# Kernel optimization log

Hardware: AMD Instinct MI355X
Metric: run time of the kernel (lower is better)

The kernel has to match this reference:

```python
import jax, jax.numpy as jnp
import numpy as np

SIZE = 1024
SIZE_INTERNAL = 4096
B, S = 8, 2048
EPS = 1e-5


def layer_norm(x, g, b):
    mu = jnp.mean(x, axis=-1, keepdims=True)
    var = jnp.mean(jnp.square(x - mu), axis=-1, keepdims=True)
    return (x - mu) * jax.lax.rsqrt(var + EPS) * g + b


def setup_inputs() -> dict:
    key = jax.random.key(0)
    ks = jax.random.split(key, 12)
    s = 0.02
    return {
        "x": jax.random.normal(ks[0], (B, S, SIZE), jnp.float32),
        "Wq": jax.random.normal(ks[1], (SIZE, SIZE), jnp.float32) * s,
        "bq": jnp.zeros((SIZE,), jnp.float32),
        "Wk": jax.random.normal(ks[2], (SIZE, SIZE), jnp.float32) * s,
        "bk": jnp.zeros((SIZE,), jnp.float32),
        "Wv": jax.random.normal(ks[3], (SIZE, SIZE), jnp.float32) * s,
        "bv": jnp.zeros((SIZE,), jnp.float32),
        "W1": jax.random.normal(ks[4], (SIZE, SIZE_INTERNAL), jnp.float32) * s,
        "b1": jnp.zeros((SIZE_INTERNAL,), jnp.float32),
        "W2": jax.random.normal(ks[5], (SIZE_INTERNAL, SIZE), jnp.float32) * s,
        "b2": jnp.zeros((SIZE,), jnp.float32),
        "g1": jnp.ones((SIZE,), jnp.float32),
        "beta1": jnp.zeros((SIZE,), jnp.float32),
        "g2": jnp.ones((SIZE,), jnp.float32),
        "beta2": jnp.zeros((SIZE,), jnp.float32),
    }


def reference(x, Wq, bq, Wk, bk, Wv, bv, W1, b1, W2, b2, g1, beta1, g2, beta2):
    # QKV projections (single-head; bmm on 3D tensors in original)
    q = x @ Wq + bq  # (B,S,d)
    k = x @ Wk + bk
    v = x @ Wv + bv
    scale = 1.0 / jnp.sqrt(jnp.asarray(SIZE, x.dtype))
    scores = jnp.einsum("bqd,bkd->bqk", q, k) * scale  # (B,S,S)
    # decoder=True -> causal mask
    causal = jnp.tril(jnp.ones((S, S), bool))
    scores = jnp.where(causal, scores, jnp.asarray(-jnp.inf, x.dtype))
    attn = jax.nn.softmax(scores, axis=-1)
    attn_out = jnp.einsum("bqk,bkd->bqd", attn, v)
    attn_out = layer_norm(attn_out, g1, beta1)
    h = jax.nn.gelu(attn_out @ W1 + b1, approximate=False)
    out = h @ W2 + b2 + attn_out
    return layer_norm(out, g2, beta2)
```

## Files before the change

kernel.cpp:

```cpp
#include <hip/hip_runtime.h>
#include <cstdint>

#define DEV __device__ __forceinline__

typedef __attribute__((ext_vector_type(8))) short bf16x8;
typedef __attribute__((ext_vector_type(4))) float f32x4;
typedef unsigned short u16;
typedef unsigned int   u32;

DEV u16 f2bf(float f) {
  u32 u = __float_as_uint(f);
  u = (u + 0x7FFFu + ((u >> 16) & 1u)) >> 16;
  return (u16)u;
}
DEV float bf2f(u16 s) { return __uint_as_float(((u32)s) << 16); }

DEV float gelu_f(float x) {
  const float ax = fabsf(x) * 0.70710678118654752f;
  const float t = 1.f / fmaf(0.3275911f, ax, 1.f);
  float p = fmaf(1.061405429f, t, -1.453152027f);
  p = fmaf(p, t, 1.421413741f);
  p = fmaf(p, t, -0.284496736f);
  p = fmaf(p, t, 0.254829592f);
  p *= t;
  const float er = 1.f - p * __expf(-ax * ax);
  const float erfx = copysignf(er, x);
  return 0.5f * x * (1.f + erfx);
}

DEV void gload_lds16(const void* g, void* l) {
  typedef __attribute__((address_space(1))) const unsigned int GU;
  typedef __attribute__((address_space(3))) unsigned int LU;
  __builtin_amdgcn_global_load_lds((GU*)(uintptr_t)g, (LU*)(u32)(uintptr_t)l, 16, 0, 0);
}

DEV int swz(int x) { return x ^ (((x >> 7) & 7) << 4); }

#define BATCH_SC 2228224L

template<int MODE>
__global__ __launch_bounds__(256, 4)
void gemm_bt(const u16* __restrict__ A, int lda, long abst,
             const u16* __restrict__ Bt, int ldb, long bbst,
             void* __restrict__ Cv, int ldc, long cbst,
             const float* __restrict__ bias,
             const float* __restrict__ bias2,
             const float* __restrict__ bias3,
             const u16* __restrict__ resid,
             int K, float scale)
{
  const int nt = blockIdx.x, mt = blockIdx.y, bz = blockIdx.z;
  if (MODE == 1 && nt > mt) return;
  const int Keff = (MODE == 2) ? (mt + 1) * 128 : K;

  __shared__ u16 As[128 * 64];
  __shared__ u16 Bs[128 * 64];

  const int tid  = threadIdx.x;
  const int lane = tid & 63;
  const int wv   = tid >> 6;
  const int wr   = wv >> 1, wc = wv & 1;
  const int lrow = lane & 15;
  const int kgrp = lane >> 4;
  const int m0 = mt * 128, n0 = nt * 128;

  const int srow = tid >> 3;
  const int scol = (tid & 7) * 8;
  const u16* Ag;
  if (MODE == 2) {
    Ag = A + bz * BATCH_SC + (long)(mt * (mt + 1) / 2) * 16384 + srow * 128 + scol;
  } else {
    Ag = A + (long)bz * abst + (long)(m0 + srow) * lda + scol;
  }
  const u16* Bg = Bt + (long)bz * bbst + (long)(n0 + srow) * ldb + scol;
  char* AsW = (char*)As + wv * 1024;
  char* BsW = (char*)Bs + wv * 1024;

  f32x4 acc[4][4];
#pragma unroll
  for (int mi = 0; mi < 4; ++mi)
#pragma unroll
    for (int ni = 0; ni < 4; ++ni)
#pragma unroll
      for (int e = 0; e < 4; ++e) acc[mi][ni][e] = 0.f;

  for (int k0 = 0; k0 < Keff; k0 += 64) {
#pragma unroll
    for (int i = 0; i < 4; ++i) {
      if (MODE == 2)
        gload_lds16(Ag + (long)(k0 >> 7) * 16384 + (k0 & 127) + i * 32 * 128, AsW + i * 4096);
      else
        gload_lds16(Ag + k0 + (long)i * 32 * lda, AsW + i * 4096);
      gload_lds16(Bg + k0 + (long)i * 32 * ldb, BsW + i * 4096);
    }
    __syncthreads();
#pragma unroll
    for (int kk = 0; kk < 2; ++kk) {
      const int kof = kk * 32 + kgrp * 8;
      bf16x8 af[4], bfr[4];
#pragma unroll
      for (int mi = 0; mi < 4; ++mi)
        af[mi] = *(const bf16x8*)&As[(wr * 64 + mi * 16 + lrow) * 64 + kof];
#pragma unroll
      for (int ni = 0; ni < 4; ++ni)
        bfr[ni] = *(const bf16x8*)&Bs[(wc * 64 + ni * 16 + lrow) * 64 + kof];
#pragma unroll
      for (int mi = 0; mi < 4; ++mi)
#pragma unroll
        for (int ni = 0; ni < 4; ++ni)
          acc[mi][ni] = __builtin_amdgcn_mfma_f32_16x16x32_bf16(af[mi], bfr[ni], acc[mi][ni], 0, 0, 0);
    }
    __syncthreads();
  }

#pragma unroll
  for (int mi = 0; mi < 4; ++mi) {
#pragma unroll
    for (int ni = 0; ni < 4; ++ni) {
#pragma unroll
      for (int e = 0; e < 4; ++e) {
        const int rr = wr * 64 + mi * 16 + kgrp * 4 + e;
        const int cc = wc * 64 + ni * 16 + lrow;
        const int gr = m0 + rr, gc = n0 + cc;
        const float v = acc[mi][ni][e];
        if (MODE == 0) {
          const float bval = gc < 1024 ? bias[gc]
                              : (gc < 2048 ? bias2[gc & 1023] : bias3[gc & 1023]);
          ((u16*)Cv)[(long)(gc >> 10) * 16777216 + (long)gr * 1024 + (gc & 1023)]
              = f2bf(v + bval);
        } else if (MODE == 1) {
          ((u16*)Cv)[bz * BATCH_SC + (long)(mt * (mt + 1) / 2 + nt) * 16384 + rr * 128 + cc]
              = f2bf(v * scale);
        } else if (MODE == 2) {
          ((float*)Cv)[(long)bz * cbst + (long)gr * ldc + gc] = v;
        } else if (MODE == 3) {
          ((u16*)Cv)[(long)gr * ldc + gc] = f2bf(gelu_f(v + bias[gc]));
        }
      }
    }
  }
}

template<int PASS>
__global__ __launch_bounds__(512, 2)
void gemm256_p8_ffn2(const u16* __restrict__ A, int lda,
                     const u16* __restrict__ Bt, int ldb,
                     float* __restrict__ Cv, int ldc,
                     const float* __restrict__ bias,
                     const u16* __restrict__ resid,
                     int K, int NNT)
{
  __shared__ char smem[131072];
  const int tid  = threadIdx.x;
  const int lane = tid & 63;
  const int wv   = tid >> 6;
  const int wm   = wv >> 2, wn = wv & 3;
  const int lrow = lane & 15;
  const int kgrp = lane >> 4;

  const int nwg = gridDim.x;
  const int q0 = nwg >> 3, r = nwg & 7, xc = blockIdx.x & 7, pos = blockIdx.x >> 3;
  const int s = (xc < r ? xc * (q0 + 1) : r * (q0 + 1) + (xc - r) * q0) + pos;
  const int mt = s / NNT, nt = s % NNT;
  const int m0 = mt * 256, n0 = nt * 256;

  auto stageA = [&](int ktile, int dslot, int h) {
    int k0 = ktile << 6; const int kmax = K - 64; if (k0 > kmax) k0 = kmax;
#pragma unroll
    for (int j = 0; j < 2; ++j) {
      const int o = j * 8192 + tid * 16;
      const int l = swz(o);
      gload_lds16(A + (long)(m0 + h * 128 + (l >> 7)) * lda + k0 + ((l & 127) >> 1),
                  smem + dslot * 65536 + h * 16384 + o);
    }
  };
  auto stageB = [&](int ktile, int dslot, int h) {
    int k0 = ktile << 6; const int kmax = K - 64; if (k0 > kmax) k0 = kmax;
#pragma unroll
    for (int j = 0; j < 2; ++j) {
      const int o = j * 8192 + tid * 16;
      const int l = swz(o);
      gload_lds16(Bt + (long)(n0 + h * 128 + (l >> 7)) * ldb + k0 + ((l & 127) >> 1),
                  smem + dslot * 65536 + 32768 + h * 16384 + o);
    }
  };
  auto rdfrag = [&](int bofs, int row, int ks) -> bf16x8 {
    const int p = swz(row * 128 + ks * 64 + kgrp * 16);
    return *(const bf16x8*)(smem + bofs + p);
  };

  f32x4 acc[8][4];
#pragma unroll
  for (int mi = 0; mi < 8; ++mi)
#pragma unroll
    for (int ni = 0; ni < 4; ++ni)
#pragma unroll
      for (int e = 0; e < 4; ++e) acc[mi][ni][e] = 0.f;

  stageA(0, 0, 0); stageA(0, 0, 1); stageB(0, 0, 0); stageB(0, 0, 1);
  stageB(1, 1, 0); stageB(1, 1, 1);
  asm volatile("s_waitcnt vmcnt(4)" ::: "memory");
  __builtin_amdgcn_s_barrier();

  const int NI = K >> 7;
  bf16x8 bfrag[4][2], afrag[2][2];
  for (int i = 0; i < NI; ++i) {
    const int kp = 2 * i;
#pragma unroll
    for (int d = 0; d < 2; ++d) {
#pragma unroll
      for (int mq = 0; mq < 4; ++mq) {
        const int ph = d * 4 + mq;
        if (mq == 0) {
#pragma unroll
          for (int ni = 0; ni < 4; ++ni)
#pragma unroll
            for (int ks = 0; ks < 2; ++ks)
              bfrag[ni][ks] = rdfrag(d * 65536 + 32768, wn * 64 + ni * 16 + lrow, ks);
        }
#pragma unroll
        for (int mi2 = 0; mi2 < 2; ++mi2)
#pragma unroll
          for (int ks = 0; ks < 2; ++ks)
            afrag[mi2][ks] = rdfrag(d * 65536, wm * 128 + (2 * mq + mi2) * 16 + lrow, ks);
        switch (ph) {
          case 0: stageA(kp + 1, 1, 0); break;
          case 1: stageA(kp + 1, 1, 1); break;
          case 2: stageB(kp + 2, 0, 0); break;
          case 3: stageB(kp + 2, 0, 1); break;
          case 4: stageA(kp + 2, 0, 0); break;
          case 5: stageA(kp + 2, 0, 1); break;
          case 6: stageB(kp + 3, 1, 0); break;
          case 7: stageB(kp + 3, 1, 1); break;
        }
        __builtin_amdgcn_s_barrier();
        asm volatile("s_waitcnt lgkmcnt(0)" ::: "memory");
        __builtin_amdgcn_s_setprio(1);
#pragma unroll
        for (int mi2 = 0; mi2 < 2; ++mi2)
#pragma unroll
          for (int ni = 0; ni < 4; ++ni)
#pragma unroll
            for (int ks = 0; ks < 2; ++ks)
              acc[2 * mq + mi2][ni] = __builtin_amdgcn_mfma_f32_16x16x32_bf16(
                  afrag[mi2][ks], bfrag[ni][ks], acc[2 * mq + mi2][ni], 0, 0, 0);
        __builtin_amdgcn_s_setprio(0);
        if (mq == 3) asm volatile("s_waitcnt vmcnt(4)" ::: "memory");
        __builtin_amdgcn_s_barrier();
      }
    }
  }

#pragma unroll
  for (int mi = 0; mi < 8; ++mi) {
#pragma unroll
    for (int ni = 0; ni < 4; ++ni) {
      const int gc = n0 + wn * 64 + ni * 16 + lrow;
#pragma unroll
      for (int e = 0; e < 4; ++e) {
        const int gr = m0 + wm * 128 + mi * 16 + kgrp * 4 + e;
        if (PASS == 0) {
          Cv[(long)gr * ldc + gc] = acc[mi][ni][e];
        } else {
          float* o = &Cv[(long)gr * ldc + gc];
          *o = *o + acc[mi][ni][e] + bias[gc] + bf2f(resid[(long)gr * 1024 + gc]);
        }
      }
    }
  }
}

template<int INBF>
__global__ __launch_bounds__(256)
void transpose_bf16(const void* __restrict__ inv, u16* __restrict__ out,
                    int R, int C, long ibst, long obst)
{
  __shared__ float t[32][33];
  const int bz = blockIdx.z;
  const int c0 = blockIdx.x * 32, r0 = blockIdx.y * 32;
  const int tx = threadIdx.x & 31, ty = threadIdx.x >> 5;
#pragma unroll
  for (int i = 0; i < 32; i += 8) {
    const long idx = (long)bz * ibst + (long)(r0 + ty + i) * C + (c0 + tx);
    t[ty + i][tx] = INBF ? bf2f(((const u16*)inv)[idx]) : ((const float*)inv)[idx];
  }
  __syncthreads();
#pragma unroll
  for (int i = 0; i < 32; i += 8)
    out[(long)bz * obst + (long)(c0 + ty + i) * R + (r0 + tx)] = f2bf(t[tx][ty + i]);
}

__global__ __launch_bounds__(256)
void cvt_f32_to_bf16(const float* __restrict__ in, u16* __restrict__ out, long n)
{
  const long idx = ((long)blockIdx.x * 256 + threadIdx.x) * 4;
  if (idx >= n) return;
  const float4 v = *(const float4*)(in + idx);
  ushort4 o;
  o.x = f2bf(v.x); o.y = f2bf(v.y); o.z = f2bf(v.z); o.w = f2bf(v.w);
  *(ushort4*)(out + idx) = o;
}

__global__ __launch_bounds__(256)
void softmax_packed(u16* __restrict__ sc)
{
  const int rowid = blockIdx.x;
  const int b = rowid >> 11, i = rowid & 2047;
  const int mtt = i >> 7, rr = i & 127;
  u16* base = sc + (long)b * BATCH_SC + (long)(mtt * (mtt + 1) / 2) * 16384 + (long)rr * 128;
  const int t = threadIdx.x;
  const int lane = t & 63, wv = t >> 6;
  const int c   = t >> 4;
  const int off = (t & 15) * 8;
  const bool act = (c <= mtt);
  const int lim = (c < mtt) ? 8 : (c == mtt ? (rr - off + 1) : 0);
  u16* p = base + (long)c * 16384 + off;

  bf16x8 vv = {};
  if (act) vv = *(const bf16x8*)p;
  float vals[8];
  float m = -1e30f;
#pragma unroll
  for (int e = 0; e < 8; ++e) {
    vals[e] = (e < lim) ? bf2f((u16)vv[e]) : -1e30f;
    m = fmaxf(m, vals[e]);
  }
#pragma unroll
  for (int o = 1; o < 64; o <<= 1) m = fmaxf(m, __shfl_xor(m, o));
  __shared__ float rm[4], rsm[4];
  if (lane == 0) rm[wv] = m;
  __syncthreads();
  m = fmaxf(fmaxf(rm[0], rm[1]), fmaxf(rm[2], rm[3]));
  float pv[8];
  float ssum = 0.f;
#pragma unroll
  for (int e = 0; e < 8; ++e) { pv[e] = __expf(vals[e] - m); ssum += pv[e]; }
#pragma unroll
  for (int o = 1; o < 64; o <<= 1) ssum += __shfl_xor(ssum, o);
  if (lane == 0) rsm[wv] = ssum;
  __syncthreads();
  ssum = rsm[0] + rsm[1] + rsm[2] + rsm[3];
  const float inv = 1.f / ssum;
  if (act) {
    bf16x8 o;
#pragma unroll
    for (int e = 0; e < 8; ++e) o[e] = (short)f2bf(pv[e] * inv);
    *(bf16x8*)p = o;
  }
}

template<int OUTBF>
__global__ __launch_bounds__(256)
void layernorm_k(const float* __restrict__ in, const float* __restrict__ gam,
                 const float* __restrict__ bet, void* __restrict__ outv)
{
  const long row = blockIdx.x;
  const int t = threadIdx.x;
  const int lane = t & 63, wv = t >> 6;
  const float4 v = ((const float4*)(in + row * 1024))[t];
  float s = v.x + v.y + v.z + v.w;
  float q = v.x * v.x + v.y * v.y + v.z * v.z + v.w * v.w;
#pragma unroll
  for (int o = 1; o < 64; o <<= 1) { s += __shfl_xor(s, o); q += __shfl_xor(q, o); }
  __shared__ float rs[4], rq[4];
  if (lane == 0) { rs[wv] = s; rq[wv] = q; }
  __syncthreads();
  s = rs[0] + rs[1] + rs[2] + rs[3];
  q = rq[0] + rq[1] + rq[2] + rq[3];
  const float mean = s * (1.f / 1024.f);
  const float var  = q * (1.f / 1024.f) - mean * mean;
  const float rstd = rsqrtf(var + 1e-5f);
  const float4 g4 = ((const float4*)gam)[t];
  const float4 b4 = ((const float4*)bet)[t];
  const float o0 = (v.x - mean) * rstd * g4.x + b4.x;
  const float o1 = (v.y - mean) * rstd * g4.y + b4.y;
  const float o2 = (v.z - mean) * rstd * g4.z + b4.z;
  const float o3 = (v.w - mean) * rstd * g4.w + b4.w;
  if (OUTBF) {
    ushort4 o; o.x = f2bf(o0); o.y = f2bf(o1); o.z = f2bf(o2); o.w = f2bf(o3);
    ((ushort4*)outv)[row * 256 + t] = o;
  } else {
    ((float4*)outv)[row * 256 + t] = make_float4(o0, o1, o2, o3);
  }
}

extern "C" void kernel_launch(void* const* d_in, const int* in_sizes, int n_in,
                              void* d_out, int out_size, void* d_ws, size_t ws_size,
                              hipStream_t stream)
{
  const float* x   = (const float*)d_in[0];
  const float* Wq  = (const float*)d_in[1];
  const float* bq  = (const float*)d_in[2];
  const float* Wk  = (const float*)d_in[3];
  const float* bk  = (const float*)d_in[4];
  const float* Wv  = (const float*)d_in[5];
  const float* bv  = (const float*)d_in[6];
  const float* W1  = (const float*)d_in[7];
  const float* b1  = (const float*)d_in[8];
  const float* W2  = (const float*)d_in[9];
  const float* b2  = (const float*)d_in[10];
  const float* g1  = (const float*)d_in[11];
  const float* be1 = (const float*)d_in[12];
  const float* g2  = (const float*)d_in[13];
  const float* be2 = (const float*)d_in[14];

  char* ws = (char*)d_ws;
  u16*   xb    = (u16*)(ws);
  u16*   vt    = xb;
  u16*   qkv   = (u16*)(ws + 33554432);
  u16*   qbuf  = qkv;
  u16*   kbuf  = qkv + 16777216;
  u16*   vbuf  = qkv + 33554432;
  u16*   ln1   = qbuf;
  u16*   hbuf  = kbuf;
  u16*   sc    = (u16*)(ws + 100663296);
  u16*   wqkvT = (u16*)(ws + 136314880);
  u16*   w1T   = (u16*)(ws + 142606336);
  u16*   w2T   = (u16*)(ws + 150994944);
  float* attnf = (float*)d_out;

  const dim3 B256(256);

  cvt_f32_to_bf16<<<dim3(16384), B256, 0, stream>>>(x, xb, 16777216L);

  transpose_bf16<0><<<dim3(32, 32, 1),  B256, 0, stream>>>(Wq, wqkvT,           1024, 1024, 0, 0);
  transpose_bf16<0><<<dim3(32, 32, 1),  B256, 0, stream>>>(Wk, wqkvT + 1048576, 1024, 1024, 0, 0);
  transpose_bf16<0><<<dim3(32, 32, 1),  B256, 0, stream>>>(Wv, wqkvT + 2097152, 1024, 1024, 0, 0);
  transpose_bf16<0><<<dim3(128, 32, 1), B256, 0, stream>>>(W1, w1T, 1024, 4096, 0, 0);
  transpose_bf16<0><<<dim3(32, 128, 1), B256, 0, stream>>>(W2, w2T, 4096, 1024, 0, 0);

  gemm_bt<0><<<dim3(24, 128), B256, 0, stream>>>(xb, 1024, 0, wqkvT, 1024, 0, qkv, 1024, 0,
                                                 bq, bk, bv, nullptr, 1024, 1.f);

  transpose_bf16<1><<<dim3(32, 64, 8), B256, 0, stream>>>(vbuf, vt, 2048, 1024, 2097152, 2097152);

  gemm_bt<1><<<dim3(16, 16, 8), B256, 0, stream>>>(qbuf, 1024, 2097152, kbuf, 1024, 2097152,
                                                   sc, 0, 0, nullptr, nullptr, nullptr, nullptr,
                                                   1024, 0.03125f);

  softmax_packed<<<dim3(16384), B256, 0, stream>>>(sc);

  gemm_bt<2><<<dim3(8, 16, 8), B256, 0, stream>>>(sc, 0, 0, vt, 2048, 2097152,
                                                  attnf, 1024, 2097152, nullptr, nullptr, nullptr,
                                                  nullptr, 0, 1.f);

  layernorm_k<1><<<dim3(16384), B256, 0, stream>>>(attnf, g1, be1, ln1);

  for (int j = 0; j < 2; ++j) {
    const u16* w1h = w1T + (long)j * 2048 * 1024;
    gemm_bt<3><<<dim3(16, 128), B256, 0, stream>>>(ln1, 1024, 0, w1h, 1024, 0, hbuf, 2048, 0,
                                                   b1 + j * 2048, nullptr, nullptr, nullptr,
                                                   1024, 1.f);
    if (j == 0)
      gemm256_p8_ffn2<0><<<dim3(256), dim3(512), 0, stream>>>(hbuf, 2048, w2T, 4096,
                                                              (float*)d_out, 1024,
                                                              nullptr, nullptr, 2048, 4);
    else
      gemm256_p8_ffn2<1><<<dim3(256), dim3(512), 0, stream>>>(hbuf, 2048, w2T + 2048, 4096,
                                                              (float*)d_out, 1024,
                                                              b2, ln1, 2048, 4);
  }

  layernorm_k<0><<<dim3(16384), B256, 0, stream>>>((float*)d_out, g2, be2, d_out);
}
```

Baseline: 745.3 us.

## Store PV output as bf16 and run FFN unchunked when workspace allows

```diff
diff --git a/kernel.cpp b/kernel.cpp
--- a/kernel.cpp
+++ b/kernel.cpp
@@ -24,8 +24,7 @@
   p = fmaf(p, t, 0.254829592f);
   p *= t;
   const float er = 1.f - p * __expf(-ax * ax);
-  const float erfx = copysignf(er, x);
-  return 0.5f * x * (1.f + erfx);
+  return 0.5f * x * (1.f + copysignf(er, x));
 }
 
 DEV void gload_lds16(const void* g, void* l) {
@@ -46,7 +45,6 @@
              const float* __restrict__ bias,
              const float* __restrict__ bias2,
              const float* __restrict__ bias3,
-             const u16* __restrict__ resid,
              int K, float scale)
 {
   const int nt = blockIdx.x, mt = blockIdx.y, bz = blockIdx.z;
@@ -132,7 +130,7 @@
           ((u16*)Cv)[bz * BATCH_SC + (long)(mt * (mt + 1) / 2 + nt) * 16384 + rr * 128 + cc]
               = f2bf(v * scale);
         } else if (MODE == 2) {
-          ((float*)Cv)[(long)bz * cbst + (long)gr * ldc + gc] = v;
+          ((u16*)Cv)[(long)bz * cbst + (long)gr * ldc + gc] = f2bf(v);
         } else if (MODE == 3) {
           ((u16*)Cv)[(long)gr * ldc + gc] = f2bf(gelu_f(v + bias[gc]));
         }
@@ -261,9 +259,12 @@
         const int gr = m0 + wm * 128 + mi * 16 + kgrp * 4 + e;
         if (PASS == 0) {
           Cv[(long)gr * ldc + gc] = acc[mi][ni][e];
-        } else {
+        } else if (PASS == 1) {
           float* o = &Cv[(long)gr * ldc + gc];
           *o = *o + acc[mi][ni][e] + bias[gc] + bf2f(resid[(long)gr * 1024 + gc]);
+        } else {
+          Cv[(long)gr * ldc + gc] = acc[mi][ni][e] + bias[gc]
+                                    + bf2f(resid[(long)gr * 1024 + gc]);
         }
       }
     }
@@ -349,17 +350,24 @@
   }
 }
 
-template<int OUTBF>
+template<int INBF, int OUTBF>
 __global__ __launch_bounds__(256)
-void layernorm_k(const float* __restrict__ in, const float* __restrict__ gam,
+void layernorm_k(const void* __restrict__ in, const float* __restrict__ gam,
                  const float* __restrict__ bet, void* __restrict__ outv)
 {
   const long row = blockIdx.x;
   const int t = threadIdx.x;
   const int lane = t & 63, wv = t >> 6;
-  const float4 v = ((const float4*)(in + row * 1024))[t];
-  float s = v.x + v.y + v.z + v.w;
-  float q = v.x * v.x + v.y * v.y + v.z * v.z + v.w * v.w;
+  float v0, v1, v2, v3;
+  if (INBF) {
+    const ushort4 u = ((const ushort4*)in)[row * 256 + t];
+    v0 = bf2f(u.x); v1 = bf2f(u.y); v2 = bf2f(u.z); v3 = bf2f(u.w);
+  } else {
+    const float4 v = ((const float4*)in)[row * 256 + t];
+    v0 = v.x; v1 = v.y; v2 = v.z; v3 = v.w;
+  }
+  float s = v0 + v1 + v2 + v3;
+  float q = v0 * v0 + v1 * v1 + v2 * v2 + v3 * v3;
 #pragma unroll
   for (int o = 1; o < 64; o <<= 1) { s += __shfl_xor(s, o); q += __shfl_xor(q, o); }
   __shared__ float rs[4], rq[4];
@@ -372,10 +380,10 @@
   const float rstd = rsqrtf(var + 1e-5f);
   const float4 g4 = ((const float4*)gam)[t];
   const float4 b4 = ((const float4*)bet)[t];
-  const float o0 = (v.x - mean) * rstd * g4.x + b4.x;
-  const float o1 = (v.y - mean) * rstd * g4.y + b4.y;
-  const float o2 = (v.z - mean) * rstd * g4.z + b4.z;
-  const float o3 = (v.w - mean) * rstd * g4.w + b4.w;
+  const float o0 = (v0 - mean) * rstd * g4.x + b4.x;
+  const float o1 = (v1 - mean) * rstd * g4.y + b4.y;
+  const float o2 = (v2 - mean) * rstd * g4.z + b4.z;
+  const float o3 = (v3 - mean) * rstd * g4.w + b4.w;
   if (OUTBF) {
     ushort4 o; o.x = f2bf(o0); o.y = f2bf(o1); o.z = f2bf(o2); o.w = f2bf(o3);
     ((ushort4*)outv)[row * 256 + t] = o;
@@ -405,19 +413,20 @@
   const float* be2 = (const float*)d_in[14];
 
   char* ws = (char*)d_ws;
-  u16*   xb    = (u16*)(ws);
+  u16*   wqkvT = (u16*)(ws);
+  u16*   w1T   = (u16*)(ws + 6291456);
+  u16*   w2T   = (u16*)(ws + 14680064);
+  u16*   xb    = (u16*)(ws + 23068672);
   u16*   vt    = xb;
-  u16*   qkv   = (u16*)(ws + 33554432);
+  u16*   qkv   = (u16*)(ws + 56623104);
   u16*   qbuf  = qkv;
   u16*   kbuf  = qkv + 16777216;
   u16*   vbuf  = qkv + 33554432;
   u16*   ln1   = qbuf;
+  u16*   pvout = kbuf;
+  u16*   sc    = (u16*)(ws + 123731968);
   u16*   hbuf  = kbuf;
-  u16*   sc    = (u16*)(ws + 100663296);
-  u16*   wqkvT = (u16*)(ws + 136314880);
-  u16*   w1T   = (u16*)(ws + 142606336);
-  u16*   w2T   = (u16*)(ws + 150994944);
-  float* attnf = (float*)d_out;
+  const bool big = (ws_size >= 224395264ULL);
 
   const dim3 B256(256);
 
@@ -430,36 +439,43 @@
   transpose_bf16<0><<<dim3(32, 128, 1), B256, 0, stream>>>(W2, w2T, 4096, 1024, 0, 0);
 
   gemm_bt<0><<<dim3(24, 128), B256, 0, stream>>>(xb, 1024, 0, wqkvT, 1024, 0, qkv, 1024, 0,
-                                                 bq, bk, bv, nullptr, 1024, 1.f);
+                                                 bq, bk, bv, 1024, 1.f);
 
   transpose_bf16<1><<<dim3(32, 64, 8), B256, 0, stream>>>(vbuf, vt, 2048, 1024, 2097152, 2097152);
 
   gemm_bt<1><<<dim3(16, 16, 8), B256, 0, stream>>>(qbuf, 1024, 2097152, kbuf, 1024, 2097152,
-                                                   sc, 0, 0, nullptr, nullptr, nullptr, nullptr,
+                                                   sc, 0, 0, nullptr, nullptr, nullptr,
                                                    1024, 0.03125f);
 
   softmax_packed<<<dim3(16384), B256, 0, stream>>>(sc);
 
   gemm_bt<2><<<dim3(8, 16, 8), B256, 0, stream>>>(sc, 0, 0, vt, 2048, 2097152,
-                                                  attnf, 1024, 2097152, nullptr, nullptr, nullptr,
-                                                  nullptr, 0, 1.f);
-
-  layernorm_k<1><<<dim3(16384), B256, 0, stream>>>(attnf, g1, be1, ln1);
-
-  for (int j = 0; j < 2; ++j) {
-    const u16* w1h = w1T + (long)j * 2048 * 1024;
-    gemm_bt<3><<<dim3(16, 128), B256, 0, stream>>>(ln1, 1024, 0, w1h, 1024, 0, hbuf, 2048, 0,
-                                                   b1 + j * 2048, nullptr, nullptr, nullptr,
-                                                   1024, 1.f);
-    if (j == 0)
-      gemm256_p8_ffn2<0><<<dim3(256), dim3(512), 0, stream>>>(hbuf, 2048, w2T, 4096,
-                                                              (float*)d_out, 1024,
-                                                              nullptr, nullptr, 2048, 4);
-    else
-      gemm256_p8_ffn2<1><<<dim3(256), dim3(512), 0, stream>>>(hbuf, 2048, w2T + 2048, 4096,
-                                                              (float*)d_out, 1024,
-                                                              b2, ln1, 2048, 4);
-  }
-
-  layernorm_k<0><<<dim3(16384), B256, 0, stream>>>((float*)d_out, g2, be2, d_out);
-}
+                                                  pvout, 1024, 2097152, nullptr, nullptr, nullptr,
+                                                  0, 1.f);
+
+  layernorm_k<1, 1><<<dim3(16384), B256, 0, stream>>>(pvout, g1, be1, ln1);
+
+  if (big) {
+    gemm_bt<3><<<dim3(32, 128), B256, 0, stream>>>(ln1, 1024, 0, w1T, 1024, 0, hbuf, 4096, 0,
+                                                   b1, nullptr, nullptr, 1024, 1.f);
+    gemm256_p8_ffn2<2><<<dim3(256), dim3(512), 0, stream>>>(hbuf, 4096, w2T, 4096,
+                                                            (float*)d_out, 1024,
+                                                            b2, ln1, 4096, 4);
+  } else {
+    for (int j = 0; j < 2; ++j) {
+      const u16* w1h = w1T + (long)j * 2048 * 1024;
+      gemm_bt<3><<<dim3(16, 128), B256, 0, stream>>>(ln1, 1024, 0, w1h, 1024, 0, hbuf, 2048, 0,
+                                                     b1 + j * 2048, nullptr, nullptr, 1024, 1.f);
+      if (j == 0)
+        gemm256_p8_ffn2<0><<<dim3(256), dim3(512), 0, stream>>>(hbuf, 2048, w2T, 4096,
+                                                                (float*)d_out, 1024,
+                                                                nullptr, nullptr, 2048, 4);
+      else
+        gemm256_p8_ffn2<1><<<dim3(256), dim3(512), 0, stream>>>(hbuf, 2048, w2T + 2048, 4096,
+                                                                (float*)d_out, 1024,
+                                                                b2, ln1, 2048, 4);
+    }
+  }
+
+  layernorm_k<0, 0><<<dim3(16384), B256, 0, stream>>>(d_out, g2, be2, d_out);
+}
```

After: 692.3 us. -7.1%, faster.
